# Optimization experiments

Hardware: AMD Instinct MI355X
Metric: run time of the kernel (lower is better)

Reference implementation:

```python
import jax, jax.numpy as jnp
import numpy as np

B, C, H, W = 8, 256, 128, 128
KC, VC, HEADS = 256, 256, 8


def setup_inputs() -> dict:
    key = jax.random.key(0)
    ks = jax.random.split(key, 10)
    s = 0.05
    return {
        "x": jax.random.normal(ks[0], (B, C, H, W), jnp.float32),
        "Wk": jax.random.normal(ks[1], (KC, C), jnp.float32) * s,
        "bk": jax.random.normal(ks[2], (KC,), jnp.float32) * s,
        "Wq": jax.random.normal(ks[3], (KC, C), jnp.float32) * s,
        "bq": jax.random.normal(ks[4], (KC,), jnp.float32) * s,
        "Wv": jax.random.normal(ks[5], (VC, C), jnp.float32) * s,
        "bv": jax.random.normal(ks[6], (VC,), jnp.float32) * s,
        "Wr": jax.random.normal(ks[7], (C, VC), jnp.float32) * s,
        "br": jax.random.normal(ks[8], (C,), jnp.float32) * s,
        "head_count": HEADS,
    }


def reference(x, Wk, bk, Wq, bq, Wv, bv, Wr, br, head_count):
    n, c, h, w = x.shape
    hw = h * w
    xf = x.reshape(n, c, hw)  # [n, C, S]
    # 1x1 convs == per-pixel linear projections
    keys = jnp.einsum('kc,ncs->nks', Wk, xf) + bk[None, :, None]
    queries = jnp.einsum('kc,ncs->nks', Wq, xf) + bq[None, :, None]
    values = jnp.einsum('vc,ncs->nvs', Wv, xf) + bv[None, :, None]

    dk = Wk.shape[0] // head_count
    dv = Wv.shape[0] // head_count
    # split heads along channel dim (matches torch channel slicing)
    K = jax.nn.softmax(keys.reshape(n, head_count, dk, hw), axis=-1)   # softmax over spatial
    Q = jax.nn.softmax(queries.reshape(n, head_count, dk, hw), axis=2) # softmax over key dim
    V = values.reshape(n, head_count, dv, hw)

    # context = K @ V^T : [n, h, dk, dv]
    ctx = jnp.einsum('nhks,nhvs->nhkv', K, V)
    # attended = ctx^T @ Q : [n, h, dv, S]
    att = jnp.einsum('nhkv,nhks->nhvs', ctx, Q).reshape(n, head_count * dv, h, w)

    attention = jnp.einsum('ov,nvhw->nohw', Wr, att) + br[None, :, None, None]
    # attention map: per-head mean over key dim, then mean over heads
    attention_map = K.mean(axis=2).mean(axis=1).reshape(n, h, w)
    # torch returns the LAST head's context (loop variable after the loop)
    context_last = ctx[:, -1]
    return attention, context_last, attention_map
```

## Files before the change

kernel.cpp:

```cpp
#include <hip/hip_runtime.h>
#include <hip/hip_bf16.h>

typedef float f32x4 __attribute__((ext_vector_type(4)));
typedef short s16x8 __attribute__((ext_vector_type(8)));
typedef __bf16 bf16x8 __attribute__((ext_vector_type(8)));
typedef unsigned short u16;

#define DEVI __device__ __forceinline__

static constexpr int    HW      = 16384;
static constexpr size_t BSTRIDE = (size_t)256 * HW;

static constexpr size_t oXBT   = 0;
static constexpr size_t oKEYS  = oXBT  + (size_t)8 * HW * 256 * 2;
static constexpr size_t oQS    = oKEYS + (size_t)8 * 256 * HW * 2;
static constexpr size_t oVB    = oQS   + (size_t)8 * 256 * HW * 2;
static constexpr size_t oWK    = oVB   + (size_t)8 * 256 * HW * 2;
static constexpr size_t oBIAS  = oWK   + (size_t)768 * 256 * 2;
static constexpr size_t oISE   = oBIAS + 4096;
static constexpr size_t oCTX   = oISE  + 8192;
static constexpr size_t oMB    = oCTX  + (size_t)64 * 1024 * 4;
static constexpr size_t oCPART = oMB   + (size_t)8 * 256 * 256 * 2;
static constexpr size_t oMPART = oCPART + (size_t)4096 * 1024 * 4;

DEVI float bf2f(short x) {
  unsigned u = ((unsigned)(unsigned short)x) << 16;
  return __builtin_bit_cast(float, u);
}
DEVI u16 f2bf(float x) { return __builtin_bit_cast(u16, (__bf16)x); }

DEVI void gld16(const void* g, void* l) {
  __builtin_amdgcn_global_load_lds(
      (__attribute__((address_space(1))) void*)(g),
      (__attribute__((address_space(3))) void*)(l), 16, 0, 0);
}

__global__ __launch_bounds__(256) void k_prep(
    const float* __restrict__ Wk, const float* __restrict__ Wq, const float* __restrict__ Wv,
    const float* __restrict__ bk, const float* __restrict__ bq, const float* __restrict__ bv,
    u16* __restrict__ Wkqv, float* __restrict__ bias)
{
  int i = blockIdx.x * 256 + threadIdx.x;
  for (int p = i; p < 768 * 256; p += 64 * 256) {
    float v = (p < 65536) ? Wk[p] : (p < 131072 ? Wq[p - 65536] : Wv[p - 131072]);
    Wkqv[p] = f2bf(v);
  }
  if (i < 768) bias[i] = (i < 256) ? bk[i] : (i < 512 ? bq[i - 256] : bv[i - 512]);
}

template<int F32IN>
__global__ __launch_bounds__(256) void k_transpose(const void* __restrict__ in_, u16* __restrict__ out)
{
  __shared__ u16 lds[64 * 256];
  const int t = threadIdx.x;
  const int n = blockIdx.y;
  const int s0 = blockIdx.x * 64;
  if constexpr (F32IN) {
    const float* src = (const float*)in_ + ((size_t)n * 256 + t) * HW + s0;
    #pragma unroll
    for (int i = 0; i < 16; ++i) {
      f32x4 v = *(const f32x4*)(src + i * 4);
      #pragma unroll
      for (int j = 0; j < 4; ++j) lds[(i * 4 + j) * 256 + t] = f2bf(v[j]);
    }
  } else {
    const u16* src = (const u16*)in_ + ((size_t)n * 256 + t) * HW + s0;
    #pragma unroll
    for (int i = 0; i < 8; ++i) {
      s16x8 v = *(const s16x8*)(src + i * 8);
      #pragma unroll
      for (int j = 0; j < 8; ++j) lds[(i * 8 + j) * 256 + t] = (u16)v[j];
    }
  }
  __syncthreads();
  s16x8* gp = (s16x8*)(out + (size_t)n * BSTRIDE + (size_t)s0 * 256);
  const s16x8* lp = (const s16x8*)lds;
  #pragma unroll
  for (int i = 0; i < 8; ++i) gp[t + i * 256] = lp[t + i * 256];
}

template<int MODE>
__global__ __launch_bounds__(256) void k_gemm(
    const u16* __restrict__ A, long a_bstride,
    const u16* __restrict__ Bt,
    const float* __restrict__ bias,
    void* __restrict__ Out)
{
  __shared__ u16 Al[2][4096];
  __shared__ u16 Bl[2][4096];
  const int t = threadIdx.x;
  const int n = blockIdx.z;
  const int m0 = blockIdx.y * 128;
  const int s0 = blockIdx.x * 128;
  const int lane = t & 63;
  const int l15 = lane & 15, l4 = lane >> 4;
  const int wv = t >> 6;
  const int wm = (wv & 1) * 64, wn = (wv >> 1) * 64;
  const u16* Ab = A + (size_t)n * a_bstride + (size_t)m0 * 256;
  const u16* Bb = Bt + (size_t)n * BSTRIDE + (size_t)s0 * 256;
  const int ar = t >> 2, ac = (t & 3) * 8;

  f32x4 acc[4][4] = {};

  auto stage = [&](int buf, int k0) {
    gld16(Ab + (size_t)ar * 256 + k0 + ac,        &Al[buf][t * 8]);
    gld16(Ab + (size_t)(ar + 64) * 256 + k0 + ac, &Al[buf][2048 + t * 8]);
    gld16(Bb + (size_t)ar * 256 + k0 + ac,        &Bl[buf][t * 8]);
    gld16(Bb + (size_t)(ar + 64) * 256 + k0 + ac, &Bl[buf][2048 + t * 8]);
  };

  stage(0, 0);
  __syncthreads();
  #pragma unroll
  for (int kt = 0; kt < 8; ++kt) {
    const int buf = kt & 1;
    if (kt < 7) stage(buf ^ 1, (kt + 1) * 32);
    bf16x8 af[4], bff[4];
    #pragma unroll
    for (int g = 0; g < 4; ++g) {
      af[g]  = *(const bf16x8*)&Al[buf][(wm + g * 16 + l15) * 32 + l4 * 8];
      bff[g] = *(const bf16x8*)&Bl[buf][(wn + g * 16 + l15) * 32 + l4 * 8];
    }
    #pragma unroll
    for (int mg = 0; mg < 4; ++mg)
      #pragma unroll
      for (int ng = 0; ng < 4; ++ng)
        acc[mg][ng] = __builtin_amdgcn_mfma_f32_16x16x32_bf16(af[mg], bff[ng], acc[mg][ng], 0, 0, 0);
    __syncthreads();
  }

  #pragma unroll
  for (int mg = 0; mg < 4; ++mg)
    #pragma unroll
    for (int r = 0; r < 4; ++r) {
      const float bb = bias[m0 + wm + mg * 16 + l4 * 4 + r];
      #pragma unroll
      for (int ng = 0; ng < 4; ++ng) acc[mg][ng][r] += bb;
    }

  if constexpr (MODE == 1) {
    #pragma unroll
    for (int hh = 0; hh < 2; ++hh)
      #pragma unroll
      for (int ng = 0; ng < 4; ++ng) {
        float s = 0.f;
        #pragma unroll
        for (int mg = hh * 2; mg < hh * 2 + 2; ++mg)
          #pragma unroll
          for (int r = 0; r < 4; ++r) { const float e = __expf(acc[mg][ng][r]); acc[mg][ng][r] = e; s += e; }
        s += __shfl_xor(s, 16);
        s += __shfl_xor(s, 32);
        const float inv = 1.f / s;
        #pragma unroll
        for (int mg = hh * 2; mg < hh * 2 + 2; ++mg)
          #pragma unroll
          for (int r = 0; r < 4; ++r) acc[mg][ng][r] *= inv;
      }
  }

  if constexpr (MODE == 2) {
    float* O = (float*)Out + (size_t)n * BSTRIDE;
    #pragma unroll
    for (int mg = 0; mg < 4; ++mg)
      #pragma unroll
      for (int r = 0; r < 4; ++r) {
        const size_t row = m0 + wm + mg * 16 + l4 * 4 + r;
        float* op = O + row * HW + s0 + wn + l15;
        #pragma unroll
        for (int ng = 0; ng < 4; ++ng) op[ng * 16] = acc[mg][ng][r];
      }
  } else {
    u16* O = (u16*)Out + (size_t)n * BSTRIDE;
    #pragma unroll
    for (int mg = 0; mg < 4; ++mg)
      #pragma unroll
      for (int r = 0; r < 4; ++r) {
        const size_t row = m0 + wm + mg * 16 + l4 * 4 + r;
        u16* op = O + row * HW + s0 + wn + l15;
        #pragma unroll
        for (int ng = 0; ng < 4; ++ng) op[ng * 16] = f2bf(acc[mg][ng][r]);
      }
  }
}

__global__ __launch_bounds__(256) void k_rowsum(const u16* __restrict__ keys, float* __restrict__ inv_se)
{
  const int k = blockIdx.x, n = blockIdx.y, t = threadIdx.x;
  const u16* row = keys + ((size_t)n * 256 + k) * HW;
  float s = 0.f;
  #pragma unroll
  for (int i = 0; i < 8; ++i) {
    s16x8 v = *(const s16x8*)(row + t * 8 + i * 2048);
    #pragma unroll
    for (int j = 0; j < 8; ++j) s += __expf(bf2f(v[j]));
  }
  #pragma unroll
  for (int m = 1; m < 64; m <<= 1) s += __shfl_xor(s, m);
  __shared__ float red[4];
  if ((t & 63) == 0) red[t >> 6] = s;
  __syncthreads();
  if (t == 0) inv_se[n * 256 + k] = 1.f / (red[0] + red[1] + red[2] + red[3]);
}

__global__ __launch_bounds__(64) void k_ctx_part(
    const u16* __restrict__ keys, const u16* __restrict__ vbuf, float* __restrict__ cpart)
{
  const int blk = blockIdx.x;
  const int chunk = blk & 63, nh = blk >> 6;
  const int h = nh & 7, n = nh >> 3;
  const int lane = threadIdx.x;
  const int l15 = lane & 15, l4 = lane >> 4;
  const u16* kb = keys + ((size_t)n * 256 + h * 32) * HW;
  const u16* vv = vbuf + ((size_t)n * 256 + h * 32) * HW;
  f32x4 acc[2][2] = {};
  const int sbase = chunk * 256 + l4 * 8;
  #pragma unroll
  for (int ks = 0; ks < 8; ++ks) {
    const int sb = sbase + ks * 32;
    bf16x8 ef[2], vf[2];
    #pragma unroll
    for (int g = 0; g < 2; ++g) {
      s16x8 kv = *(const s16x8*)(kb + (size_t)(g * 16 + l15) * HW + sb);
      bf16x8 e;
      #pragma unroll
      for (int j = 0; j < 8; ++j) e[j] = (__bf16)__expf(bf2f(kv[j]));
      ef[g] = e;
      vf[g] = *(const bf16x8*)(vv + (size_t)(g * 16 + l15) * HW + sb);
    }
    #pragma unroll
    for (int a = 0; a < 2; ++a)
      #pragma unroll
      for (int b = 0; b < 2; ++b)
        acc[a][b] = __builtin_amdgcn_mfma_f32_16x16x32_bf16(ef[a], vf[b], acc[a][b], 0, 0, 0);
  }
  float* op = cpart + (size_t)blk * 1024;
  #pragma unroll
  for (int a = 0; a < 2; ++a)
    #pragma unroll
    for (int b = 0; b < 2; ++b)
      #pragma unroll
      for (int r = 0; r < 4; ++r)
        op[(a * 16 + l4 * 4 + r) * 32 + b * 16 + l15] = acc[a][b][r];
}

__global__ __launch_bounds__(256) void k_ctx_reduce(
    const float* __restrict__ cpart, const float* __restrict__ inv_se,
    float* __restrict__ ctx, float* __restrict__ dctx)
{
  const int nh = blockIdx.x, n = nh >> 3, h = nh & 7, t = threadIdx.x;
  f32x4 a = {};
  for (int c = 0; c < 64; ++c) a += *(const f32x4*)(cpart + ((size_t)nh * 64 + c) * 1024 + t * 4);
  const float inv = inv_se[n * 256 + h * 32 + (t >> 3)];
  a *= inv;
  *(f32x4*)(ctx + (size_t)nh * 1024 + t * 4) = a;
  if (h == 7) *(f32x4*)(dctx + (size_t)n * 1024 + t * 4) = a;
}

__global__ __launch_bounds__(256) void k_mmat(
    const float* __restrict__ ctx, const float* __restrict__ Wr, u16* __restrict__ Mb)
{
  const int nh = blockIdx.x, n = nh >> 3, h = nh & 7, o = threadIdx.x;
  __shared__ float cl[1024];
  #pragma unroll
  for (int i = 0; i < 4; ++i) cl[o + i * 256] = ctx[(size_t)nh * 1024 + o + i * 256];
  __syncthreads();
  float wr[32];
  const float* wp = Wr + (size_t)o * 256 + h * 32;
  #pragma unroll
  for (int v = 0; v < 32; ++v) wr[v] = wp[v];
  u16* mp = Mb + ((size_t)n * 256 + o) * 256 + h * 32;
  #pragma unroll 4
  for (int k = 0; k < 32; ++k) {
    float s = 0.f;
    #pragma unroll
    for (int v = 0; v < 32; ++v) s += wr[v] * cl[k * 32 + v];
    mp[k] = f2bf(s);
  }
}

__global__ __launch_bounds__(64) void k_map_part(
    const u16* __restrict__ keys, const float* __restrict__ inv_se, float* __restrict__ mpart)
{
  const int st = blockIdx.x, kq = blockIdx.y, n = blockIdx.z, t = threadIdx.x;
  const int s0 = st * 512 + t * 8;
  const u16* kb = keys + (size_t)n * 256 * HW;
  const float* ip = inv_se + n * 256 + kq * 64;
  f32x4 a[2] = {};
  #pragma unroll 4
  for (int kk = 0; kk < 64; ++kk) {
    const int k = kq * 64 + kk;
    const float iv = ip[kk];
    s16x8 v = *(const s16x8*)(kb + (size_t)k * HW + s0);
    #pragma unroll
    for (int j = 0; j < 8; ++j) a[j >> 2][j & 3] += __expf(bf2f(v[j])) * iv;
  }
  float* mp = mpart + ((size_t)kq * 8 + n) * HW + s0;
  *(f32x4*)mp = a[0];
  *(f32x4*)(mp + 4) = a[1];
}

__global__ __launch_bounds__(256) void k_map_reduce(const float* __restrict__ mpart, float* __restrict__ dmap)
{
  const int i = blockIdx.x * 256 + threadIdx.x;
  f32x4 a = {};
  #pragma unroll
  for (int kq = 0; kq < 4; ++kq) a += *(const f32x4*)(mpart + (size_t)kq * 131072 + (size_t)i * 4);
  a *= (1.0f / 256.0f);
  *(f32x4*)(dmap + (size_t)i * 4) = a;
}

extern "C" void kernel_launch(void* const* d_in, const int* in_sizes, int n_in,
                              void* d_out, int out_size, void* d_ws, size_t ws_size,
                              hipStream_t stream)
{
  (void)in_sizes; (void)n_in; (void)out_size; (void)ws_size;
  const float* x  = (const float*)d_in[0];
  const float* Wk = (const float*)d_in[1];
  const float* bk = (const float*)d_in[2];
  const float* Wq = (const float*)d_in[3];
  const float* bq = (const float*)d_in[4];
  const float* Wv = (const float*)d_in[5];
  const float* bv = (const float*)d_in[6];
  const float* Wr = (const float*)d_in[7];
  const float* br = (const float*)d_in[8];

  char* ws = (char*)d_ws;
  u16*   xbT  = (u16*)(ws + oXBT);
  u16*   keys = (u16*)(ws + oKEYS);
  u16*   qs   = (u16*)(ws + oQS);
  u16*   vbuf = (u16*)(ws + oVB);
  u16*   Wkqv = (u16*)(ws + oWK);
  float* bias = (float*)(ws + oBIAS);
  float* ise  = (float*)(ws + oISE);
  float* ctx  = (float*)(ws + oCTX);
  u16*   Mb   = (u16*)(ws + oMB);
  float* cpart= (float*)(ws + oCPART);
  float* mpart= (float*)(ws + oMPART);

  float* attn = (float*)d_out;
  float* dctx = (float*)d_out + 33554432;
  float* dmap = (float*)d_out + 33562624;

  k_prep<<<64, 256, 0, stream>>>(Wk, Wq, Wv, bk, bq, bv, Wkqv, bias);
  k_transpose<1><<<dim3(256, 8), 256, 0, stream>>>(x, xbT);
  k_gemm<0><<<dim3(128, 2, 8), 256, 0, stream>>>(Wkqv,             0, xbT, bias,       keys);
  k_gemm<1><<<dim3(128, 2, 8), 256, 0, stream>>>(Wkqv + 256 * 256, 0, xbT, bias + 256, qs);
  k_gemm<0><<<dim3(128, 2, 8), 256, 0, stream>>>(Wkqv + 512 * 256, 0, xbT, bias + 512, vbuf);
  k_rowsum<<<dim3(256, 8), 256, 0, stream>>>(keys, ise);
  k_ctx_part<<<4096, 64, 0, stream>>>(keys, vbuf, cpart);
  k_ctx_reduce<<<64, 256, 0, stream>>>(cpart, ise, ctx, dctx);
  k_mmat<<<64, 256, 0, stream>>>(ctx, Wr, Mb);
  k_map_part<<<dim3(32, 4, 8), 64, 0, stream>>>(keys, ise, mpart);
  k_map_reduce<<<128, 256, 0, stream>>>(mpart, dmap);
  k_transpose<0><<<dim3(256, 8), 256, 0, stream>>>(qs, xbT);
  k_gemm<2><<<dim3(128, 2, 8), 256, 0, stream>>>(Mb, 256 * 256, xbT, br, attn);
}
```

Before: 309.3 us.

## Fuse K/Q/V projections into one GEMM with fused exp, rowsum and transposed Q epilogues

Merges the three projection GEMMs into a single launch that computes exp(keys) and per-tile partial row sums, writes softmaxed Q already transposed through LDS, and stores V. This removes the separate rowsum pass, the bf16 Q transpose kernel and the map_part pass. The attention-map accumulation moves into the context kernel, which reuses the exp-keys loads it already makes. Risks include storing exp(keys) in bf16 before normalisation, a larger partial-sum buffer with a serial reduce kernel, and more branching in the GEMM epilogue.

```diff
diff --git a/kernel.cpp b/kernel.cpp
--- a/kernel.cpp
+++ b/kernel.cpp
@@ -12,13 +12,14 @@
 static constexpr size_t BSTRIDE = (size_t)256 * HW;
 
 static constexpr size_t oXBT   = 0;
-static constexpr size_t oKEYS  = oXBT  + (size_t)8 * HW * 256 * 2;
-static constexpr size_t oQS    = oKEYS + (size_t)8 * 256 * HW * 2;
-static constexpr size_t oVB    = oQS   + (size_t)8 * 256 * HW * 2;
+static constexpr size_t oEK    = oXBT  + (size_t)8 * HW * 256 * 2;
+static constexpr size_t oQT    = oEK   + (size_t)8 * 256 * HW * 2;
+static constexpr size_t oVB    = oQT   + (size_t)8 * HW * 256 * 2;
 static constexpr size_t oWK    = oVB   + (size_t)8 * 256 * HW * 2;
 static constexpr size_t oBIAS  = oWK   + (size_t)768 * 256 * 2;
 static constexpr size_t oISE   = oBIAS + 4096;
-static constexpr size_t oCTX   = oISE  + 8192;
+static constexpr size_t oPS    = oISE  + 8192;
+static constexpr size_t oCTX   = oPS   + (size_t)256 * 2048 * 4;
 static constexpr size_t oMB    = oCTX  + (size_t)64 * 1024 * 4;
 static constexpr size_t oCPART = oMB   + (size_t)8 * 256 * 256 * 2;
 static constexpr size_t oMPART = oCPART + (size_t)4096 * 1024 * 4;
@@ -48,29 +49,18 @@
   if (i < 768) bias[i] = (i < 256) ? bk[i] : (i < 512 ? bq[i - 256] : bv[i - 512]);
 }
 
-template<int F32IN>
-__global__ __launch_bounds__(256) void k_transpose(const void* __restrict__ in_, u16* __restrict__ out)
+__global__ __launch_bounds__(256) void k_transpose(const float* __restrict__ in_, u16* __restrict__ out)
 {
   __shared__ u16 lds[64 * 256];
   const int t = threadIdx.x;
   const int n = blockIdx.y;
   const int s0 = blockIdx.x * 64;
-  if constexpr (F32IN) {
-    const float* src = (const float*)in_ + ((size_t)n * 256 + t) * HW + s0;
-    #pragma unroll
-    for (int i = 0; i < 16; ++i) {
-      f32x4 v = *(const f32x4*)(src + i * 4);
-      #pragma unroll
-      for (int j = 0; j < 4; ++j) lds[(i * 4 + j) * 256 + t] = f2bf(v[j]);
-    }
-  } else {
-    const u16* src = (const u16*)in_ + ((size_t)n * 256 + t) * HW + s0;
-    #pragma unroll
-    for (int i = 0; i < 8; ++i) {
-      s16x8 v = *(const s16x8*)(src + i * 8);
-      #pragma unroll
-      for (int j = 0; j < 8; ++j) lds[(i * 8 + j) * 256 + t] = (u16)v[j];
-    }
+  const float* src = in_ + ((size_t)n * 256 + t) * HW + s0;
+  #pragma unroll
+  for (int i = 0; i < 16; ++i) {
+    f32x4 v = *(const f32x4*)(src + i * 4);
+    #pragma unroll
+    for (int j = 0; j < 4; ++j) lds[(i * 4 + j) * 256 + t] = f2bf(v[j]);
   }
   __syncthreads();
   s16x8* gp = (s16x8*)(out + (size_t)n * BSTRIDE + (size_t)s0 * 256);
@@ -79,25 +69,279 @@
   for (int i = 0; i < 8; ++i) gp[t + i * 256] = lp[t + i * 256];
 }
 
-template<int MODE>
-__global__ __launch_bounds__(256) void k_gemm(
-    const u16* __restrict__ A, long a_bstride,
-    const u16* __restrict__ Bt,
-    const float* __restrict__ bias,
-    void* __restrict__ Out)
-{
-  __shared__ u16 Al[2][4096];
-  __shared__ u16 Bl[2][4096];
+__global__ __launch_bounds__(256) void k_proj(
+    const u16* __restrict__ W, const u16* __restrict__ xbT, const float* __restrict__ bias,
+    u16* __restrict__ ek, u16* __restrict__ qT, u16* __restrict__ vb, float* __restrict__ ps)
+{
+  __shared__ u16 smem[17408];
+  u16* Al = smem;
+  u16* Bl = smem + 8192;
   const int t = threadIdx.x;
-  const int n = blockIdx.z;
-  const int m0 = blockIdx.y * 128;
-  const int s0 = blockIdx.x * 128;
+  const int L = blockIdx.x;
+  const int n  = L & 7;
+  const int idx = L >> 3;
+  const int mb = idx % 6;
+  const int sb = idx / 6;
+  const int m0 = mb * 128, s0 = sb * 128;
   const int lane = t & 63;
   const int l15 = lane & 15, l4 = lane >> 4;
   const int wv = t >> 6;
   const int wm = (wv & 1) * 64, wn = (wv >> 1) * 64;
-  const u16* Ab = A + (size_t)n * a_bstride + (size_t)m0 * 256;
-  const u16* Bb = Bt + (size_t)n * BSTRIDE + (size_t)s0 * 256;
+  const u16* Ab = W + (size_t)m0 * 256;
+  const u16* Bb = xbT + (size_t)n * BSTRIDE + (size_t)s0 * 256;
+  const int ar = t >> 2, ac = (t & 3) * 8;
+
+  f32x4 acc[4][4] = {};
+
+  auto stage = [&](int buf, int k0) {
+    gld16(Ab + (size_t)ar * 256 + k0 + ac,        Al + buf * 4096 + t * 8);
+    gld16(Ab + (size_t)(ar + 64) * 256 + k0 + ac, Al + buf * 4096 + 2048 + t * 8);
+    gld16(Bb + (size_t)ar * 256 + k0 + ac,        Bl + buf * 4096 + t * 8);
+    gld16(Bb + (size_t)(ar + 64) * 256 + k0 + ac, Bl + buf * 4096 + 2048 + t * 8);
+  };
+
+  stage(0, 0);
+  __syncthreads();
+  #pragma unroll
+  for (int kt = 0; kt < 8; ++kt) {
+    const int buf = kt & 1;
+    if (kt < 7) stage(buf ^ 1, (kt + 1) * 32);
+    bf16x8 af[4], bff[4];
+    #pragma unroll
+    for (int g = 0; g < 4; ++g) {
+      af[g]  = *(const bf16x8*)&Al[buf * 4096 + (wm + g * 16 + l15) * 32 + l4 * 8];
+      bff[g] = *(const bf16x8*)&Bl[buf * 4096 + (wn + g * 16 + l15) * 32 + l4 * 8];
+    }
+    #pragma unroll
+    for (int mg = 0; mg < 4; ++mg)
+      #pragma unroll
+      for (int ng = 0; ng < 4; ++ng)
+        acc[mg][ng] = __builtin_amdgcn_mfma_f32_16x16x32_bf16(af[mg], bff[ng], acc[mg][ng], 0, 0, 0);
+    __syncthreads();
+  }
+
+  #pragma unroll
+  for (int mg = 0; mg < 4; ++mg)
+    #pragma unroll
+    for (int r = 0; r < 4; ++r) {
+      const float bb = bias[m0 + wm + mg * 16 + l4 * 4 + r];
+      #pragma unroll
+      for (int ng = 0; ng < 4; ++ng) acc[mg][ng][r] += bb;
+    }
+
+  const int rowBase = (mb & 1) * 128;
+
+  if (mb < 2) {
+    #pragma unroll
+    for (int mg = 0; mg < 4; ++mg)
+      #pragma unroll
+      for (int r = 0; r < 4; ++r) {
+        float s_ = 0.f;
+        #pragma unroll
+        for (int ng = 0; ng < 4; ++ng) {
+          const float e = __expf(acc[mg][ng][r]);
+          acc[mg][ng][r] = e; s_ += e;
+        }
+        s_ += __shfl_xor(s_, 1); s_ += __shfl_xor(s_, 2);
+        s_ += __shfl_xor(s_, 4); s_ += __shfl_xor(s_, 8);
+        if (l15 == 0) {
+          const int row = rowBase + wm + mg * 16 + l4 * 4 + r;
+          ps[((size_t)(sb * 2 + (wn >> 6))) * 2048 + n * 256 + row] = s_;
+        }
+      }
+    u16* O = ek + (size_t)n * BSTRIDE;
+    #pragma unroll
+    for (int mg = 0; mg < 4; ++mg)
+      #pragma unroll
+      for (int r = 0; r < 4; ++r) {
+        const size_t row = rowBase + wm + mg * 16 + l4 * 4 + r;
+        u16* op = O + row * HW + s0 + wn + l15;
+        #pragma unroll
+        for (int ng = 0; ng < 4; ++ng) op[ng * 16] = f2bf(acc[mg][ng][r]);
+      }
+  } else if (mb < 4) {
+    #pragma unroll
+    for (int hh = 0; hh < 2; ++hh)
+      #pragma unroll
+      for (int ng = 0; ng < 4; ++ng) {
+        float s = 0.f;
+        #pragma unroll
+        for (int mg = hh * 2; mg < hh * 2 + 2; ++mg)
+          #pragma unroll
+          for (int r = 0; r < 4; ++r) { const float e = __expf(acc[mg][ng][r]); acc[mg][ng][r] = e; s += e; }
+        s += __shfl_xor(s, 16);
+        s += __shfl_xor(s, 32);
+        const float inv = 1.f / s;
+        #pragma unroll
+        for (int mg = hh * 2; mg < hh * 2 + 2; ++mg)
+          #pragma unroll
+          for (int r = 0; r < 4; ++r) acc[mg][ng][r] *= inv;
+      }
+    #pragma unroll
+    for (int mg = 0; mg < 4; ++mg)
+      #pragma unroll
+      for (int ng = 0; ng < 4; ++ng)
+        #pragma unroll
+        for (int r = 0; r < 4; ++r) {
+          const int srow = wn + ng * 16 + l15;
+          const int mcol = wm + mg * 16 + l4 * 4 + r;
+          smem[srow * 136 + mcol] = f2bf(acc[mg][ng][r]);
+        }
+    __syncthreads();
+    u16* O = qT + (size_t)n * BSTRIDE + (size_t)s0 * 256 + rowBase;
+    #pragma unroll
+    for (int it = 0; it < 8; ++it) {
+      const int row = it * 16 + (t >> 4);
+      *(s16x8*)(O + (size_t)row * 256 + (t & 15) * 8) = *(const s16x8*)&smem[row * 136 + (t & 15) * 8];
+    }
+  } else {
+    u16* O = vb + (size_t)n * BSTRIDE;
+    #pragma unroll
+    for (int mg = 0; mg < 4; ++mg)
+      #pragma unroll
+      for (int r = 0; r < 4; ++r) {
+        const size_t row = rowBase + wm + mg * 16 + l4 * 4 + r;
+        u16* op = O + row * HW + s0 + wn + l15;
+        #pragma unroll
+        for (int ng = 0; ng < 4; ++ng) op[ng * 16] = f2bf(acc[mg][ng][r]);
+      }
+  }
+}
+
+__global__ __launch_bounds__(256) void k_inv(const float* __restrict__ ps, float* __restrict__ ise)
+{
+  const int i = blockIdx.x * 256 + threadIdx.x;
+  float s = 0.f;
+  for (int b = 0; b < 256; ++b) s += ps[(size_t)b * 2048 + i];
+  ise[i] = 1.f / s;
+}
+
+__global__ __launch_bounds__(64) void k_ctx_part(
+    const u16* __restrict__ ek, const u16* __restrict__ vb, const float* __restrict__ ise,
+    float* __restrict__ cpart, float* __restrict__ mpart)
+{
+  const int blk = blockIdx.x;
+  const int chunk = blk & 63, nh = blk >> 6;
+  const int h = nh & 7, n = nh >> 3;
+  const int lane = threadIdx.x;
+  const int l15 = lane & 15, l4 = lane >> 4;
+  const u16* kb = ek + ((size_t)n * 256 + h * 32) * HW;
+  const u16* vv = vb + ((size_t)n * 256 + h * 32) * HW;
+  const float iv0 = ise[n * 256 + h * 32 + l15];
+  const float iv1 = ise[n * 256 + h * 32 + 16 + l15];
+  f32x4 acc[2][2] = {};
+  float macc[8][8] = {};
+  const int sbase = chunk * 256 + l4 * 8;
+  #pragma unroll
+  for (int ks = 0; ks < 8; ++ks) {
+    const int sb = sbase + ks * 32;
+    bf16x8 ef[2], vf[2];
+    #pragma unroll
+    for (int g = 0; g < 2; ++g) {
+      ef[g] = *(const bf16x8*)(kb + (size_t)(g * 16 + l15) * HW + sb);
+      vf[g] = *(const bf16x8*)(vv + (size_t)(g * 16 + l15) * HW + sb);
+    }
+    #pragma unroll
+    for (int j = 0; j < 8; ++j)
+      macc[ks][j] = fmaf(iv0, (float)ef[0][j], fmaf(iv1, (float)ef[1][j], macc[ks][j]));
+    #pragma unroll
+    for (int a = 0; a < 2; ++a)
+      #pragma unroll
+      for (int b = 0; b < 2; ++b)
+        acc[a][b] = __builtin_amdgcn_mfma_f32_16x16x32_bf16(ef[a], vf[b], acc[a][b], 0, 0, 0);
+  }
+  float* op = cpart + (size_t)blk * 1024;
+  #pragma unroll
+  for (int a = 0; a < 2; ++a)
+    #pragma unroll
+    for (int b = 0; b < 2; ++b)
+      #pragma unroll
+      for (int r = 0; r < 4; ++r)
+        op[(a * 16 + l4 * 4 + r) * 32 + b * 16 + l15] = acc[a][b][r];
+  #pragma unroll
+  for (int ks = 0; ks < 8; ++ks)
+    #pragma unroll
+    for (int j = 0; j < 8; ++j) {
+      float v = macc[ks][j];
+      v += __shfl_xor(v, 1); v += __shfl_xor(v, 2);
+      v += __shfl_xor(v, 4); v += __shfl_xor(v, 8);
+      macc[ks][j] = v;
+    }
+  if (l15 == 0) {
+    float* mp = mpart + ((size_t)h * 8 + n) * HW + sbase;
+    #pragma unroll
+    for (int ks = 0; ks < 8; ++ks) {
+      f32x4 a = {macc[ks][0], macc[ks][1], macc[ks][2], macc[ks][3]};
+      f32x4 b = {macc[ks][4], macc[ks][5], macc[ks][6], macc[ks][7]};
+      *(f32x4*)(mp + ks * 32)     = a;
+      *(f32x4*)(mp + ks * 32 + 4) = b;
+    }
+  }
+}
+
+__global__ __launch_bounds__(256) void k_ctx_reduce(
+    const float* __restrict__ cpart, const float* __restrict__ ise,
+    float* __restrict__ ctx, float* __restrict__ dctx)
+{
+  const int nh = blockIdx.x, n = nh >> 3, h = nh & 7, t = threadIdx.x;
+  f32x4 a = {};
+  for (int c = 0; c < 64; ++c) a += *(const f32x4*)(cpart + ((size_t)nh * 64 + c) * 1024 + t * 4);
+  const float inv = ise[n * 256 + h * 32 + (t >> 3)];
+  a *= inv;
+  *(f32x4*)(ctx + (size_t)nh * 1024 + t * 4) = a;
+  if (h == 7) *(f32x4*)(dctx + (size_t)n * 1024 + t * 4) = a;
+}
+
+__global__ __launch_bounds__(256) void k_mmat(
+    const float* __restrict__ ctx, const float* __restrict__ Wr, u16* __restrict__ Mb)
+{
+  const int nh = blockIdx.x, n = nh >> 3, h = nh & 7, o = threadIdx.x;
+  __shared__ float cl[1024];
+  #pragma unroll
+  for (int i = 0; i < 4; ++i) cl[o + i * 256] = ctx[(size_t)nh * 1024 + o + i * 256];
+  __syncthreads();
+  float wr[32];
+  const float* wp = Wr + (size_t)o * 256 + h * 32;
+  #pragma unroll
+  for (int v = 0; v < 32; ++v) wr[v] = wp[v];
+  u16* mp = Mb + ((size_t)n * 256 + o) * 256 + h * 32;
+  #pragma unroll 4
+  for (int k = 0; k < 32; ++k) {
+    float s = 0.f;
+    #pragma unroll
+    for (int v = 0; v < 32; ++v) s += wr[v] * cl[k * 32 + v];
+    mp[k] = f2bf(s);
+  }
+}
+
+__global__ __launch_bounds__(256) void k_map_reduce(const float* __restrict__ mpart, float* __restrict__ dmap)
+{
+  const int i = blockIdx.x * 256 + threadIdx.x;
+  f32x4 a = {};
+  #pragma unroll
+  for (int h = 0; h < 8; ++h) a += *(const f32x4*)(mpart + (size_t)h * 131072 + (size_t)i * 4);
+  a *= (1.0f / 256.0f);
+  *(f32x4*)(dmap + (size_t)i * 4) = a;
+}
+
+__global__ __launch_bounds__(256) void k_attn(
+    const u16* __restrict__ Mb, const u16* __restrict__ qT, const float* __restrict__ br,
+    float* __restrict__ Out)
+{
+  __shared__ u16 Al[2][4096];
+  __shared__ u16 Bl[2][4096];
+  const int t = threadIdx.x;
+  const int L = blockIdx.x;
+  const int n = L & 7;
+  const int idx = L >> 3;
+  const int m0 = (idx & 1) * 128;
+  const int s0 = (idx >> 1) * 128;
+  const int lane = t & 63;
+  const int l15 = lane & 15, l4 = lane >> 4;
+  const int wv = t >> 6;
+  const int wm = (wv & 1) * 64, wn = (wv >> 1) * 64;
+  const u16* Ab = Mb + (size_t)n * 65536 + (size_t)m0 * 256;
+  const u16* Bb = qT + (size_t)n * BSTRIDE + (size_t)s0 * 256;
   const int ar = t >> 2, ac = (t & 3) * 8;
 
   f32x4 acc[4][4] = {};
@@ -129,184 +373,17 @@
     __syncthreads();
   }
 
+  float* O = Out + (size_t)n * BSTRIDE;
   #pragma unroll
   for (int mg = 0; mg < 4; ++mg)
     #pragma unroll
     for (int r = 0; r < 4; ++r) {
-      const float bb = bias[m0 + wm + mg * 16 + l4 * 4 + r];
-      #pragma unroll
-      for (int ng = 0; ng < 4; ++ng) acc[mg][ng][r] += bb;
-    }
-
-  if constexpr (MODE == 1) {
-    #pragma unroll
-    for (int hh = 0; hh < 2; ++hh)
-      #pragma unroll
-      for (int ng = 0; ng < 4; ++ng) {
-        float s = 0.f;
-        #pragma unroll
-        for (int mg = hh * 2; mg < hh * 2 + 2; ++mg)
-          #pragma unroll
-          for (int r = 0; r < 4; ++r) { const float e = __expf(acc[mg][ng][r]); acc[mg][ng][r] = e; s += e; }
-        s += __shfl_xor(s, 16);
-        s += __shfl_xor(s, 32);
-        const float inv = 1.f / s;
-        #pragma unroll
-        for (int mg = hh * 2; mg < hh * 2 + 2; ++mg)
-          #pragma unroll
-          for (int r = 0; r < 4; ++r) acc[mg][ng][r] *= inv;
-      }
-  }
-
-  if constexpr (MODE == 2) {
-    float* O = (float*)Out + (size_t)n * BSTRIDE;
-    #pragma unroll
-    for (int mg = 0; mg < 4; ++mg)
-      #pragma unroll
-      for (int r = 0; r < 4; ++r) {
-        const size_t row = m0 + wm + mg * 16 + l4 * 4 + r;
-        float* op = O + row * HW + s0 + wn + l15;
-        #pragma unroll
-        for (int ng = 0; ng < 4; ++ng) op[ng * 16] = acc[mg][ng][r];
-      }
-  } else {
-    u16* O = (u16*)Out + (size_t)n * BSTRIDE;
-    #pragma unroll
-    for (int mg = 0; mg < 4; ++mg)
-      #pragma unroll
-      for (int r = 0; r < 4; ++r) {
-        const size_t row = m0 + wm + mg * 16 + l4 * 4 + r;
-        u16* op = O + row * HW + s0 + wn + l15;
-        #pragma unroll
-        for (int ng = 0; ng < 4; ++ng) op[ng * 16] = f2bf(acc[mg][ng][r]);
-      }
-  }
-}
-
-__global__ __launch_bounds__(256) void k_rowsum(const u16* __restrict__ keys, float* __restrict__ inv_se)
-{
-  const int k = blockIdx.x, n = blockIdx.y, t = threadIdx.x;
-  const u16* row = keys + ((size_t)n * 256 + k) * HW;
-  float s = 0.f;
-  #pragma unroll
-  for (int i = 0; i < 8; ++i) {
-    s16x8 v = *(const s16x8*)(row + t * 8 + i * 2048);
-    #pragma unroll
-    for (int j = 0; j < 8; ++j) s += __expf(bf2f(v[j]));
-  }
-  #pragma unroll
-  for (int m = 1; m < 64; m <<= 1) s += __shfl_xor(s, m);
-  __shared__ float red[4];
-  if ((t & 63) == 0) red[t >> 6] = s;
-  __syncthreads();
-  if (t == 0) inv_se[n * 256 + k] = 1.f / (red[0] + red[1] + red[2] + red[3]);
-}
-
-__global__ __launch_bounds__(64) void k_ctx_part(
-    const u16* __restrict__ keys, const u16* __restrict__ vbuf, float* __restrict__ cpart)
-{
-  const int blk = blockIdx.x;
-  const int chunk = blk & 63, nh = blk >> 6;
-  const int h = nh & 7, n = nh >> 3;
-  const int lane = threadIdx.x;
-  const int l15 = lane & 15, l4 = lane >> 4;
-  const u16* kb = keys + ((size_t)n * 256 + h * 32) * HW;
-  const u16* vv = vbuf + ((size_t)n * 256 + h * 32) * HW;
-  f32x4 acc[2][2] = {};
-  const int sbase = chunk * 256 + l4 * 8;
-  #pragma unroll
-  for (int ks = 0; ks < 8; ++ks) {
-    const int sb = sbase + ks * 32;
-    bf16x8 ef[2], vf[2];
-    #pragma unroll
-    for (int g = 0; g < 2; ++g) {
-      s16x8 kv = *(const s16x8*)(kb + (size_t)(g * 16 + l15) * HW + sb);
-      bf16x8 e;
-      #pragma unroll
-      for (int j = 0; j < 8; ++j) e[j] = (__bf16)__expf(bf2f(kv[j]));
-      ef[g] = e;
-      vf[g] = *(const bf16x8*)(vv + (size_t)(g * 16 + l15) * HW + sb);
-    }
-    #pragma unroll
-    for (int a = 0; a < 2; ++a)
-      #pragma unroll
-      for (int b = 0; b < 2; ++b)
-        acc[a][b] = __builtin_amdgcn_mfma_f32_16x16x32_bf16(ef[a], vf[b], acc[a][b], 0, 0, 0);
-  }
-  float* op = cpart + (size_t)blk * 1024;
-  #pragma unroll
-  for (int a = 0; a < 2; ++a)
-    #pragma unroll
-    for (int b = 0; b < 2; ++b)
-      #pragma unroll
-      for (int r = 0; r < 4; ++r)
-        op[(a * 16 + l4 * 4 + r) * 32 + b * 16 + l15] = acc[a][b][r];
-}
-
-__global__ __launch_bounds__(256) void k_ctx_reduce(
-    const float* __restrict__ cpart, const float* __restrict__ inv_se,
-    float* __restrict__ ctx, float* __restrict__ dctx)
-{
-  const int nh = blockIdx.x, n = nh >> 3, h = nh & 7, t = threadIdx.x;
-  f32x4 a = {};
-  for (int c = 0; c < 64; ++c) a += *(const f32x4*)(cpart + ((size_t)nh * 64 + c) * 1024 + t * 4);
-  const float inv = inv_se[n * 256 + h * 32 + (t >> 3)];
-  a *= inv;
-  *(f32x4*)(ctx + (size_t)nh * 1024 + t * 4) = a;
-  if (h == 7) *(f32x4*)(dctx + (size_t)n * 1024 + t * 4) = a;
-}
-
-__global__ __launch_bounds__(256) void k_mmat(
-    const float* __restrict__ ctx, const float* __restrict__ Wr, u16* __restrict__ Mb)
-{
-  const int nh = blockIdx.x, n = nh >> 3, h = nh & 7, o = threadIdx.x;
-  __shared__ float cl[1024];
-  #pragma unroll
-  for (int i = 0; i < 4; ++i) cl[o + i * 256] = ctx[(size_t)nh * 1024 + o + i * 256];
-  __syncthreads();
-  float wr[32];
-  const float* wp = Wr + (size_t)o * 256 + h * 32;
-  #pragma unroll
-  for (int v = 0; v < 32; ++v) wr[v] = wp[v];
-  u16* mp = Mb + ((size_t)n * 256 + o) * 256 + h * 32;
-  #pragma unroll 4
-  for (int k = 0; k < 32; ++k) {
-    float s = 0.f;
-    #pragma unroll
-    for (int v = 0; v < 32; ++v) s += wr[v] * cl[k * 32 + v];
-    mp[k] = f2bf(s);
-  }
-}
-
-__global__ __launch_bounds__(64) void k_map_part(
-    const u16* __restrict__ keys, const float* __restrict__ inv_se, float* __restrict__ mpart)
-{
-  const int st = blockIdx.x, kq = blockIdx.y, n = blockIdx.z, t = threadIdx.x;
-  const int s0 = st * 512 + t * 8;
-  const u16* kb = keys + (size_t)n * 256 * HW;
-  const float* ip = inv_se + n * 256 + kq * 64;
-  f32x4 a[2] = {};
-  #pragma unroll 4
-  for (int kk = 0; kk < 64; ++kk) {
-    const int k = kq * 64 + kk;
-    const float iv = ip[kk];
-    s16x8 v = *(const s16x8*)(kb + (size_t)k * HW + s0);
-    #pragma unroll
-    for (int j = 0; j < 8; ++j) a[j >> 2][j & 3] += __expf(bf2f(v[j])) * iv;
-  }
-  float* mp = mpart + ((size_t)kq * 8 + n) * HW + s0;
-  *(f32x4*)mp = a[0];
-  *(f32x4*)(mp + 4) = a[1];
-}
-
-__global__ __launch_bounds__(256) void k_map_reduce(const float* __restrict__ mpart, float* __restrict__ dmap)
-{
-  const int i = blockIdx.x * 256 + threadIdx.x;
-  f32x4 a = {};
-  #pragma unroll
-  for (int kq = 0; kq < 4; ++kq) a += *(const f32x4*)(mpart + (size_t)kq * 131072 + (size_t)i * 4);
-  a *= (1.0f / 256.0f);
-  *(f32x4*)(dmap + (size_t)i * 4) = a;
+      const size_t row = m0 + wm + mg * 16 + l4 * 4 + r;
+      const float bb = br[row];
+      float* op = O + row * HW + s0 + wn + l15;
+      #pragma unroll
+      for (int ng = 0; ng < 4; ++ng) op[ng * 16] = acc[mg][ng][r] + bb;
+    }
 }
 
 extern "C" void kernel_launch(void* const* d_in, const int* in_sizes, int n_in,
@@ -326,12 +403,13 @@
 
   char* ws = (char*)d_ws;
   u16*   xbT  = (u16*)(ws + oXBT);
-  u16*   keys = (u16*)(ws + oKEYS);
-  u16*   qs   = (u16*)(ws + oQS);
-  u16*   vbuf = (u16*)(ws + oVB);
+  u16*   ek   = (u16*)(ws + oEK);
+  u16*   qT   = (u16*)(ws + oQT);
+  u16*   vb   = (u16*)(ws + oVB);
   u16*   Wkqv = (u16*)(ws + oWK);
   float* bias = (float*)(ws + oBIAS);
   float* ise  = (float*)(ws + oISE);
+  float* ps   = (float*)(ws + oPS);
   float* ctx  = (float*)(ws + oCTX);
   u16*   Mb   = (u16*)(ws + oMB);
   float* cpart= (float*)(ws + oCPART);
@@ -342,16 +420,12 @@
   float* dmap = (float*)d_out + 33562624;
 
   k_prep<<<64, 256, 0, stream>>>(Wk, Wq, Wv, bk, bq, bv, Wkqv, bias);
-  k_transpose<1><<<dim3(256, 8), 256, 0, stream>>>(x, xbT);
-  k_gemm<0><<<dim3(128, 2, 8), 256, 0, stream>>>(Wkqv,             0, xbT, bias,       keys);
-  k_gemm<1><<<dim3(128, 2, 8), 256, 0, stream>>>(Wkqv + 256 * 256, 0, xbT, bias + 256, qs);
-  k_gemm<0><<<dim3(128, 2, 8), 256, 0, stream>>>(Wkqv + 512 * 256, 0, xbT, bias + 512, vbuf);
-  k_rowsum<<<dim3(256, 8), 256, 0, stream>>>(keys, ise);
-  k_ctx_part<<<4096, 64, 0, stream>>>(keys, vbuf, cpart);
+  k_transpose<<<dim3(256, 8), 256, 0, stream>>>(x, xbT);
+  k_proj<<<6144, 256, 0, stream>>>(Wkqv, xbT, bias, ek, qT, vb, ps);
+  k_inv<<<8, 256, 0, stream>>>(ps, ise);
+  k_ctx_part<<<4096, 64, 0, stream>>>(ek, vb, ise, cpart, mpart);
   k_ctx_reduce<<<64, 256, 0, stream>>>(cpart, ise, ctx, dctx);
   k_mmat<<<64, 256, 0, stream>>>(ctx, Wr, Mb);
-  k_map_part<<<dim3(32, 4, 8), 64, 0, stream>>>(keys, ise, mpart);
   k_map_reduce<<<128, 256, 0, stream>>>(mpart, dmap);
-  k_transpose<0><<<dim3(256, 8), 256, 0, stream>>>(qs, xbT);
-  k_gemm<2><<<dim3(128, 2, 8), 256, 0, stream>>>(Mb, 256 * 256, xbT, br, attn);
-}
+  k_attn<<<2048, 256, 0, stream>>>(Mb, qT, br, attn);
+}
```

Result: faster. 289.7 us (-6.3%).
